# Kernel optimization log

Measured on AMD Instinct MI355X. Metric: run time of the kernel, lower is better.

## Reference

```python
import jax, jax.numpy as jnp
import numpy as np

D_MODEL = 1024
N_HEAD = 16
AGENT_NUM = 256


def setup_inputs() -> dict:
    key = jax.random.key(0)
    ks = jax.random.split(key, 11)
    B, S, D = 4, 2048, D_MODEL
    s = 1.0 / np.sqrt(D)
    return {
        "q": jax.random.normal(ks[0], (B, S, D), jnp.float32),
        "k": jax.random.normal(ks[1], (B, S, D), jnp.float32),
        "v": jax.random.normal(ks[2], (B, S, D), jnp.float32),
        "Wq": jax.random.normal(ks[3], (D, D), jnp.float32) * s,
        "bq": jnp.zeros((D,), jnp.float32),
        "Wk": jax.random.normal(ks[4], (D, D), jnp.float32) * s,
        "bk": jnp.zeros((D,), jnp.float32),
        "Wv": jax.random.normal(ks[5], (D, D), jnp.float32) * s,
        "bv": jnp.zeros((D,), jnp.float32),
        "Wo": jax.random.normal(ks[6], (D, D), jnp.float32) * s,
        "bo": jnp.zeros((D,), jnp.float32),
    }


def _split_heads(x, n_head):
    B, S, D = x.shape
    return x.reshape(B, S, n_head, D // n_head).transpose(0, 2, 1, 3)  # [B,H,S,d]


def reference(q, k, v, Wq, bq, Wk, bk, Wv, bv, Wo, bo):
    B, S, D = q.shape
    H, A = N_HEAD, AGENT_NUM
    d = D // H
    scale = 1.0 / jnp.sqrt(jnp.asarray(d, q.dtype))

    # QKV linear projections (torch Linear: x @ W.T + b)
    qh = _split_heads(q @ Wq.T + bq, H)  # [B,H,S,d]
    kh = _split_heads(k @ Wk.T + bk, H)
    vh = _split_heads(v @ Wv.T + bv, H)

    # Agent tokens: average-pool queries along sequence down to A tokens
    agent = qh.reshape(B, H, A, S // A, d).mean(axis=3)  # [B,H,A,d]

    # Stage 1: agents aggregate from keys/values (softmax over S)
    agent_attn = jax.nn.softmax(
        jnp.einsum("bhad,bhsd->bhas", agent, kh) * scale, axis=-1)  # [B,H,A,S]
    agent_v = jnp.einsum("bhas,bhsd->bhad", agent_attn, vh)  # [B,H,A,d]

    # Stage 2: queries attend to agent tokens (softmax over A)
    q_attn = jax.nn.softmax(
        jnp.einsum("bhsd,bhad->bhsa", qh, agent) * scale, axis=-1)  # [B,H,S,A]
    out_h = jnp.einsum("bhsa,bhad->bhsd", q_attn, agent_v)  # [B,H,S,d]

    # concat heads + output projection
    out = out_h.transpose(0, 2, 1, 3).reshape(B, S, D)
    out = out @ Wo.T + bo
    return out, q_attn
```

## Files before the change

kernel.cpp:

```cpp
#include <hip/hip_runtime.h>

constexpr int Bsz = 4, Ssz = 2048, Dsz = 1024, Hn = 16, dh = 64, An = 256;

typedef __attribute__((ext_vector_type(8))) short bf16x8;
typedef __attribute__((ext_vector_type(4))) float f32x4;

__device__ __forceinline__ unsigned short f2bf_rn(float f) {
    unsigned int u = __float_as_uint(f);
    return (unsigned short)((u + 0x7FFFu + ((u >> 16) & 1u)) >> 16);
}
__device__ __forceinline__ float bf2f(unsigned short h) {
    return __uint_as_float(((unsigned int)h) << 16);
}
__device__ __forceinline__ void bf_split(float f, unsigned short& hi, unsigned short& lo) {
    hi = f2bf_rn(f);
    lo = f2bf_rn(f - bf2f(hi));
}
__device__ __forceinline__ void gload16(const unsigned short* g, unsigned short* l) {
    __builtin_amdgcn_global_load_lds(
        (const __attribute__((address_space(1))) unsigned int*)g,
        (__attribute__((address_space(3))) unsigned int*)l, 16, 0, 0);
}
__device__ __forceinline__ bf16x8 gfrag(const unsigned short* g) {
    return *reinterpret_cast<const bf16x8*>(g);
}
__device__ __forceinline__ void make8(float4 a, float4 b, bf16x8& hi8, bf16x8& lo8) {
    float v[8] = {a.x, a.y, a.z, a.w, b.x, b.y, b.z, b.w};
    #pragma unroll
    for (int i = 0; i < 8; ++i) {
        unsigned short h, l;
        bf_split(v[i], h, l);
        hi8[i] = (short)h; lo8[i] = (short)l;
    }
}


template<int LOGC, int NISS>
__device__ __forceinline__ void stage_tile(const unsigned short* __restrict__ g, long rowStride,
                                           unsigned short* lbase, int t) {
    const int wid = t >> 6;
    #pragma unroll
    for (int i = 0; i < NISS; ++i) {
        int slot = i * 256 + t;
        int r = slot >> LOGC;
        int c = slot & ((1 << LOGC) - 1);
        int cs = (c ^ (r & 7)) & ((1 << LOGC) - 1);
        gload16(g + (long)r * rowStride + cs * 8, lbase + (i * 256 + wid * 64) * 8);
    }
}
template<int ROWLEN>
__device__ __forceinline__ bf16x8 fragR(const unsigned short* buf, int row, int ks, int lane) {
    int c = ks * 4 + (lane >> 4);
    int cs = (c ^ (row & 7)) & (ROWLEN / 8 - 1);
    return *reinterpret_cast<const bf16x8*>(buf + row * ROWLEN + cs * 8);
}

__global__ __launch_bounds__(256)
void split_kernel(const float* __restrict__ x, unsigned short* __restrict__ hi,
                  unsigned short* __restrict__ lo, int n4)
{
    int i = blockIdx.x * 256 + threadIdx.x;
    if (i >= n4) return;
    float4 v = reinterpret_cast<const float4*>(x)[i];
    ushort4 h, l;
    bf_split(v.x, h.x, l.x);
    bf_split(v.y, h.y, l.y);
    bf_split(v.z, h.z, l.z);
    bf_split(v.w, h.w, l.w);
    reinterpret_cast<ushort4*>(hi)[i] = h;
    reinterpret_cast<ushort4*>(lo)[i] = l;
}

#define MT 128
#define BKm 32

__device__ __forceinline__ bf16x8 lds_frag(const unsigned short* buf, int baseRow, int lane) {
    int row = baseRow + (lane & 15);
    int c = lane >> 4;
    int idx = row * 32 + ((c ^ ((row >> 1) & 3)) << 3);
    return *reinterpret_cast<const bf16x8*>(buf + idx);
}

template<int OMODE>
__global__ __launch_bounds__(256, 2)
void gemm_nt_mfma3(const unsigned short* __restrict__ Ahi, const unsigned short* __restrict__ Alo,
                   const unsigned short* __restrict__ Bhi, const unsigned short* __restrict__ Blo,
                   const float* __restrict__ bias, float* __restrict__ Cf,
                   unsigned short* __restrict__ Chi, unsigned short* __restrict__ Clo,
                   int K, int N)
{
    __shared__ unsigned short lds[4 * 4096];
    const int t = threadIdx.x;
    const int lane = t & 63, wid = t >> 6;
    const int wr = wid >> 1, wc = wid & 1;
    const int m0 = blockIdx.y * MT, n0 = blockIdx.x * MT;

    const int srow0 = t >> 2;
    const int x4 = t & 3;
    const int ldsBase0 = (wid * 64) * 8;
    const int ldsBase1 = (256 + wid * 64) * 8;

    f32x4 acc[4][4];
    #pragma unroll
    for (int i = 0; i < 4; ++i)
        #pragma unroll
        for (int j = 0; j < 4; ++j)
            acc[i][j] = f32x4{0.f, 0.f, 0.f, 0.f};

    const unsigned short* gA[2] = {Ahi, Alo};
    const unsigned short* gB[2] = {Bhi, Blo};

    for (int k0 = 0; k0 < K; k0 += BKm) {
        #pragma unroll
        for (int hb = 0; hb < 2; ++hb) {
            {
                const unsigned short* G = gA[hb];
                int r0 = srow0, r1 = srow0 + 64;
                int c0 = x4 ^ ((r0 >> 1) & 3);
                int c1 = x4 ^ ((r1 >> 1) & 3);
                gload16(G + (size_t)(m0 + r0) * K + k0 + c0 * 8, lds + hb * 4096 + ldsBase0);
                gload16(G + (size_t)(m0 + r1) * K + k0 + c1 * 8, lds + hb * 4096 + ldsBase1);
            }
            {
                const unsigned short* G = gB[hb];
                int r0 = srow0, r1 = srow0 + 64;
                int c0 = x4 ^ ((r0 >> 1) & 3);
                int c1 = x4 ^ ((r1 >> 1) & 3);
                gload16(G + (size_t)(n0 + r0) * K + k0 + c0 * 8, lds + (2 + hb) * 4096 + ldsBase0);
                gload16(G + (size_t)(n0 + r1) * K + k0 + c1 * 8, lds + (2 + hb) * 4096 + ldsBase1);
            }
        }
        __syncthreads();

        bf16x8 ah[4], al[4], bh[4], bl[4];
        #pragma unroll
        for (int mi = 0; mi < 4; ++mi) {
            ah[mi] = lds_frag(lds + 0 * 4096, wr * 64 + mi * 16, lane);
            al[mi] = lds_frag(lds + 1 * 4096, wr * 64 + mi * 16, lane);
        }
        #pragma unroll
        for (int ni = 0; ni < 4; ++ni) {
            bh[ni] = lds_frag(lds + 2 * 4096, wc * 64 + ni * 16, lane);
            bl[ni] = lds_frag(lds + 3 * 4096, wc * 64 + ni * 16, lane);
        }
        #pragma unroll
        for (int mi = 0; mi < 4; ++mi)
            #pragma unroll
            for (int ni = 0; ni < 4; ++ni) {
                acc[mi][ni] = __builtin_amdgcn_mfma_f32_16x16x32_bf16(ah[mi], bh[ni], acc[mi][ni], 0, 0, 0);
                acc[mi][ni] = __builtin_amdgcn_mfma_f32_16x16x32_bf16(ah[mi], bl[ni], acc[mi][ni], 0, 0, 0);
                acc[mi][ni] = __builtin_amdgcn_mfma_f32_16x16x32_bf16(al[mi], bh[ni], acc[mi][ni], 0, 0, 0);
            }
        __syncthreads();
    }

    #pragma unroll
    for (int mi = 0; mi < 4; ++mi) {
        #pragma unroll
        for (int ni = 0; ni < 4; ++ni) {
            const int n = n0 + wc * 64 + ni * 16 + (lane & 15);
            const float bval = bias[n];
            #pragma unroll
            for (int j = 0; j < 4; ++j) {
                const int m = m0 + wr * 64 + mi * 16 + ((lane >> 4) << 2) + j;
                float val = acc[mi][ni][j] + bval;
                if constexpr (OMODE == 0) {
                    Cf[(size_t)m * N + n] = val;
                } else {
                    const int b = m >> 11, s = m & (Ssz - 1);
                    const int h = n >> 6, c = n & (dh - 1);
                    size_t idx;
                    if constexpr (OMODE == 1)
                        idx = (((size_t)(b * Hn + h)) * Ssz + s) * dh + c;
                    else if constexpr (OMODE == 2)
                        idx = (((size_t)(b * Hn + h)) * dh + c) * Ssz + s;
                    else
                        idx = (size_t)(b * Hn + h) * 131072
                            + (((s >> 4) * 2 + (c >> 5)) << 9)
                            + (((c >> 3) & 3) << 7) + ((s & 15) << 3) + (c & 7);
                    unsigned short hi, lo;
                    bf_split(val, hi, lo);
                    Chi[idx] = hi; Clo[idx] = lo;
                }
            }
        }
    }
}

__global__ __launch_bounds__(256)
void pool_agent(const unsigned short* __restrict__ qh_hi, const unsigned short* __restrict__ qh_lo,
                unsigned short* __restrict__ ag_hi, unsigned short* __restrict__ ag_lo)
{
    const int idx = blockIdx.x * 256 + threadIdx.x;
    const int c = idx & (dh - 1);
    const int a = (idx >> 6) & (An - 1);
    const int bh = idx >> 14;
    const size_t base = (size_t)bh * 131072
        + (((a >> 1) * 2 + (c >> 5)) << 9) + (((c >> 3) & 3) << 7)
        + ((8 * (a & 1)) << 3) + (c & 7);
    float s = 0.f;
    #pragma unroll
    for (int j = 0; j < 8; ++j)
        s += bf2f(qh_hi[base + j * 8]) + bf2f(qh_lo[base + j * 8]);
    s *= 0.125f;
    unsigned short hi, lo;
    bf_split(s, hi, lo);
    const size_t oidx = (size_t)bh * 16384
        + (((a >> 4) * 2 + (c >> 5)) << 9) + (((c >> 3) & 3) << 7)
        + ((a & 15) << 3) + (c & 7);
    ag_hi[oidx] = hi; ag_lo[oidx] = lo;
}

__global__ __launch_bounds__(256, 3)
void flash1(const unsigned short* __restrict__ ag_hi, const unsigned short* __restrict__ ag_lo,
            const unsigned short* __restrict__ kh_hi, const unsigned short* __restrict__ kh_lo,
            const unsigned short* __restrict__ vt_hi_g, const unsigned short* __restrict__ vt_lo_g,
            unsigned short* __restrict__ avt_hi, unsigned short* __restrict__ avt_lo)
{
    __shared__ unsigned short lds[24576];
    unsigned short* kth = lds;
    unsigned short* ktl = lds + 4096;
    unsigned short* vth = lds + 8192;
    unsigned short* vtl = lds + 12288;
    const int t = threadIdx.x;
    const int lane = t & 63, w = t >> 6;
    const int al15 = lane & 15, hi4 = lane >> 4;
    unsigned short* pwh = lds + 16384 + w * 2048;
    unsigned short* pwl = pwh + 1024;

    const int bh = blockIdx.y;
    const int a0 = blockIdx.x * 64;

    bf16x8 bqh[2], bql[2];
    {
        const size_t abase = (size_t)bh * 16384 + (size_t)((a0 >> 4) + w) * 1024;
        #pragma unroll
        for (int ks = 0; ks < 2; ++ks) {
            bqh[ks] = gfrag(ag_hi + abase + ks * 512 + lane * 8);
            bql[ks] = gfrag(ag_lo + abase + ks * 512 + lane * 8);
        }
    }

    f32x4 O[4];
    #pragma unroll
    for (int i = 0; i < 4; ++i) O[i] = f32x4{0.f, 0.f, 0.f, 0.f};
    float m_run = -INFINITY, l_run = 0.f;

    for (int s0 = 0; s0 < Ssz; s0 += 64) {
        stage_tile<3, 2>(kh_hi + ((size_t)bh * Ssz + s0) * dh, dh, kth, t);
        stage_tile<3, 2>(kh_lo + ((size_t)bh * Ssz + s0) * dh, dh, ktl, t);
        stage_tile<3, 2>(vt_hi_g + (size_t)bh * dh * Ssz + s0, Ssz, vth, t);
        stage_tile<3, 2>(vt_lo_g + (size_t)bh * dh * Ssz + s0, Ssz, vtl, t);
        __syncthreads();

        f32x4 sc[4];
        #pragma unroll
        for (int si = 0; si < 4; ++si) sc[si] = f32x4{0.f, 0.f, 0.f, 0.f};
        #pragma unroll
        for (int si = 0; si < 4; ++si)
            #pragma unroll
            for (int ks = 0; ks < 2; ++ks) {
                bf16x8 ah = fragR<64>(kth, si * 16 + al15, ks, lane);
                bf16x8 al = fragR<64>(ktl, si * 16 + al15, ks, lane);
                sc[si] = __builtin_amdgcn_mfma_f32_16x16x32_bf16(ah, bqh[ks], sc[si], 0, 0, 0);
                sc[si] = __builtin_amdgcn_mfma_f32_16x16x32_bf16(ah, bql[ks], sc[si], 0, 0, 0);
                sc[si] = __builtin_amdgcn_mfma_f32_16x16x32_bf16(al, bqh[ks], sc[si], 0, 0, 0);
            }

        float tmax = -INFINITY;
        #pragma unroll
        for (int si = 0; si < 4; ++si)
            #pragma unroll
            for (int j = 0; j < 4; ++j) {
                sc[si][j] *= 0.125f;
                tmax = fmaxf(tmax, sc[si][j]);
            }
        tmax = fmaxf(tmax, __shfl_xor(tmax, 16));
        tmax = fmaxf(tmax, __shfl_xor(tmax, 32));
        float newm = fmaxf(m_run, tmax);
        float fac = __expf(m_run - newm);
        float tsum = 0.f;
        #pragma unroll
        for (int si = 0; si < 4; ++si)
            #pragma unroll
            for (int j = 0; j < 4; ++j) {
                float p = __expf(sc[si][j] - newm);
                sc[si][j] = p;
                tsum += p;
            }
        tsum += __shfl_xor(tsum, 16);
        tsum += __shfl_xor(tsum, 32);
        l_run = l_run * fac + tsum;
        m_run = newm;

        #pragma unroll
        for (int si = 0; si < 4; ++si) {
            ushort4 h4, l4;
            bf_split(sc[si][0], h4.x, l4.x);
            bf_split(sc[si][1], h4.y, l4.y);
            bf_split(sc[si][2], h4.z, l4.z);
            bf_split(sc[si][3], h4.w, l4.w);
            int baseS = si * 16 + (hi4 << 2);
            int addr = al15 * 64 + (baseS ^ ((al15 & 7) << 3));
            *reinterpret_cast<ushort4*>(pwh + addr) = h4;
            *reinterpret_cast<ushort4*>(pwl + addr) = l4;
        }

        float fj[4];
        #pragma unroll
        for (int j = 0; j < 4; ++j) fj[j] = __shfl(fac, (hi4 << 2) + j);
        #pragma unroll
        for (int di = 0; di < 4; ++di)
            #pragma unroll
            for (int j = 0; j < 4; ++j) O[di][j] *= fj[j];

        #pragma unroll
        for (int ks = 0; ks < 2; ++ks) {
            bf16x8 pah = fragR<64>(pwh, al15, ks, lane);
            bf16x8 pal = fragR<64>(pwl, al15, ks, lane);
            #pragma unroll
            for (int di = 0; di < 4; ++di) {
                bf16x8 vh = fragR<64>(vth, di * 16 + al15, ks, lane);
                bf16x8 vl = fragR<64>(vtl, di * 16 + al15, ks, lane);
                O[di] = __builtin_amdgcn_mfma_f32_16x16x32_bf16(pah, vh, O[di], 0, 0, 0);
                O[di] = __builtin_amdgcn_mfma_f32_16x16x32_bf16(pah, vl, O[di], 0, 0, 0);
                O[di] = __builtin_amdgcn_mfma_f32_16x16x32_bf16(pal, vh, O[di], 0, 0, 0);
            }
        }
        __syncthreads();
    }

    float lj[4];
    #pragma unroll
    for (int j = 0; j < 4; ++j) lj[j] = __shfl(l_run, (hi4 << 2) + j);
    #pragma unroll
    for (int di = 0; di < 4; ++di) {
        ushort4 h4, l4;
        #pragma unroll
        for (int j = 0; j < 4; ++j) {
            float val = O[di][j] / lj[j];
            unsigned short hi, lo;
            bf_split(val, hi, lo);
            ((unsigned short*)&h4)[j] = hi;
            ((unsigned short*)&l4)[j] = lo;
        }
        const size_t oidx = (size_t)bh * 16384
            + (size_t)(di * 8 + (a0 >> 5) + (w >> 1)) * 512
            + (size_t)((2 * w + (hi4 >> 1)) & 3) * 128
            + al15 * 8 + (hi4 & 1) * 4;
        *reinterpret_cast<ushort4*>(avt_hi + oidx) = h4;
        *reinterpret_cast<ushort4*>(avt_lo + oidx) = l4;
    }
}

__global__ __launch_bounds__(256, 2)
void flash2(const unsigned short* __restrict__ qh_hi, const unsigned short* __restrict__ qh_lo,
            const unsigned short* __restrict__ ag_hi, const unsigned short* __restrict__ ag_lo,
            const unsigned short* __restrict__ avt_hi, const unsigned short* __restrict__ avt_lo,
            float* __restrict__ q_attn,
            unsigned short* __restrict__ xo_hi, unsigned short* __restrict__ xo_lo)
{
    __shared__ float plds[4][4096];

    const int t = threadIdx.x, lane = t & 63, w = t >> 6;
    const int al15 = lane & 15, hi4 = lane >> 4;
    const int bh = blockIdx.y;
    const int s0 = blockIdx.x * 64;
    float* P = plds[w];

    bf16x8 bqh[2], bql[2];
    {
        const size_t qbase = (size_t)bh * 131072 + (size_t)((s0 >> 4) + w) * 1024;
        #pragma unroll
        for (int ks = 0; ks < 2; ++ks) {
            bqh[ks] = gfrag(qh_hi + qbase + ks * 512 + lane * 8);
            bql[ks] = gfrag(qh_lo + qbase + ks * 512 + lane * 8);
        }
    }

    const unsigned short* agh = ag_hi + (size_t)bh * 16384;
    const unsigned short* agl = ag_lo + (size_t)bh * 16384;
    f32x4 acc[16];
    #pragma unroll
    for (int ai = 0; ai < 16; ++ai) acc[ai] = f32x4{0.f, 0.f, 0.f, 0.f};
    #pragma unroll
    for (int ai = 0; ai < 16; ++ai)
        #pragma unroll
        for (int ks = 0; ks < 2; ++ks) {
            bf16x8 ah = gfrag(agh + (ai * 2 + ks) * 512 + lane * 8);
            bf16x8 al = gfrag(agl + (ai * 2 + ks) * 512 + lane * 8);
            acc[ai] = __builtin_amdgcn_mfma_f32_16x16x32_bf16(ah, bqh[ks], acc[ai], 0, 0, 0);
            acc[ai] = __builtin_amdgcn_mfma_f32_16x16x32_bf16(ah, bql[ks], acc[ai], 0, 0, 0);
            acc[ai] = __builtin_amdgcn_mfma_f32_16x16x32_bf16(al, bqh[ks], acc[ai], 0, 0, 0);
        }

    float mx = -INFINITY;
    #pragma unroll
    for (int ai = 0; ai < 16; ++ai)
        #pragma unroll
        for (int j = 0; j < 4; ++j) {
            acc[ai][j] *= 0.125f;
            mx = fmaxf(mx, acc[ai][j]);
        }
    mx = fmaxf(mx, __shfl_xor(mx, 16));
    mx = fmaxf(mx, __shfl_xor(mx, 32));
    float sum = 0.f;
    #pragma unroll
    for (int ai = 0; ai < 16; ++ai)
        #pragma unroll
        for (int j = 0; j < 4; ++j) {
            float p = __expf(acc[ai][j] - mx);
            acc[ai][j] = p;
            sum += p;
        }
    sum += __shfl_xor(sum, 16);
    sum += __shfl_xor(sum, 32);
    const float inv = 1.0f / sum;

    #pragma unroll
    for (int ai = 0; ai < 16; ++ai) {
        float4 o;
        o.x = acc[ai][0] * inv; o.y = acc[ai][1] * inv;
        o.z = acc[ai][2] * inv; o.w = acc[ai][3] * inv;
        int pos4 = (ai * 4 + hi4) ^ (al15 & 7);
        *reinterpret_cast<float4*>(P + al15 * 256 + pos4 * 4) = o;
    }

    {
        float* qbase = q_attn + ((size_t)bh * Ssz + s0 + w * 16) * An;
        #pragma unroll
        for (int r = 0; r < 16; ++r) {
            float4 f = *reinterpret_cast<const float4*>(P + r * 256 + ((lane ^ (r & 7)) * 4));
            *reinterpret_cast<float4*>(qbase + r * An + lane * 4) = f;
        }
    }

    const unsigned short* avh_b = avt_hi + (size_t)bh * 16384;
    const unsigned short* avl_b = avt_lo + (size_t)bh * 16384;
    f32x4 O[4];
    #pragma unroll
    for (int i = 0; i < 4; ++i) O[i] = f32x4{0.f, 0.f, 0.f, 0.f};
    #pragma unroll
    for (int ks = 0; ks < 8; ++ks) {
        int p4 = ks * 8 + hi4 * 2;
        float4 fa = *reinterpret_cast<const float4*>(P + al15 * 256 + ((p4 ^ (al15 & 7)) * 4));
        float4 fb = *reinterpret_cast<const float4*>(P + al15 * 256 + (((p4 + 1) ^ (al15 & 7)) * 4));
        bf16x8 pah, pal;
        make8(fa, fb, pah, pal);
        #pragma unroll
        for (int di = 0; di < 4; ++di) {
            bf16x8 avh = gfrag(avh_b + (di * 8 + ks) * 512 + lane * 8);
            bf16x8 avl = gfrag(avl_b + (di * 8 + ks) * 512 + lane * 8);
            O[di] = __builtin_amdgcn_mfma_f32_16x16x32_bf16(pah, avh, O[di], 0, 0, 0);
            O[di] = __builtin_amdgcn_mfma_f32_16x16x32_bf16(pah, avl, O[di], 0, 0, 0);
            O[di] = __builtin_amdgcn_mfma_f32_16x16x32_bf16(pal, avh, O[di], 0, 0, 0);
        }
    }

    const int b = bh >> 4, h = bh & (Hn - 1);
    #pragma unroll
    for (int di = 0; di < 4; ++di)
        #pragma unroll
        for (int j = 0; j < 4; ++j) {
            float val = O[di][j];
            int sG = s0 + w * 16 + (hi4 << 2) + j;
            int dfull = h * dh + di * 16 + al15;
            size_t idx = ((size_t)b * Ssz + sG) * Dsz + dfull;
            unsigned short hi, lo;
            bf_split(val, hi, lo);
            xo_hi[idx] = hi; xo_lo[idx] = lo;
        }
}

extern "C" void kernel_launch(void* const* d_in, const int* in_sizes, int n_in,
                              void* d_out, int out_size, void* d_ws, size_t ws_size,
                              hipStream_t stream)
{
    const float* q  = (const float*)d_in[0];
    const float* k  = (const float*)d_in[1];
    const float* v  = (const float*)d_in[2];
    const float* Wq = (const float*)d_in[3];
    const float* bq = (const float*)d_in[4];
    const float* Wk = (const float*)d_in[5];
    const float* bk = (const float*)d_in[6];
    const float* Wv = (const float*)d_in[7];
    const float* bv = (const float*)d_in[8];
    const float* Wo = (const float*)d_in[9];
    const float* bo = (const float*)d_in[10];

    constexpr size_t BSD = (size_t)Bsz * Ssz * Dsz;
    constexpr size_t DD  = (size_t)Dsz * Dsz;
    constexpr size_t AGD = (size_t)Bsz * Hn * An * dh;

    float* out    = (float*)d_out;
    float* q_attn = out + BSD;

    unsigned short* u = (unsigned short*)d_ws;
    unsigned short* x_hi   = u;
    unsigned short* x_lo   = x_hi + BSD;
    unsigned short* qh_hi  = x_lo + BSD;
    unsigned short* qh_lo  = qh_hi + BSD;
    unsigned short* kh_hi  = qh_lo + BSD;
    unsigned short* kh_lo  = kh_hi + BSD;
    unsigned short* vt_hi  = kh_lo + BSD;
    unsigned short* vt_lo  = vt_hi + BSD;
    unsigned short* w_hi   = vt_lo + BSD;
    unsigned short* w_lo   = w_hi + DD;
    unsigned short* ag_hi  = w_lo + DD;
    unsigned short* ag_lo  = ag_hi + AGD;
    unsigned short* avt_hi = ag_lo + AGD;
    unsigned short* avt_lo = avt_hi + AGD;

    const int M = Bsz * Ssz;
    dim3 gmfma(Dsz / MT, M / MT, 1);

    split_kernel<<<BSD / 1024, 256, 0, stream>>>(q, x_hi, x_lo, BSD / 4);
    split_kernel<<<DD / 1024, 256, 0, stream>>>(Wq, w_hi, w_lo, DD / 4);
    gemm_nt_mfma3<3><<<gmfma, 256, 0, stream>>>(x_hi, x_lo, w_hi, w_lo, bq, nullptr, qh_hi, qh_lo, Dsz, Dsz);
    split_kernel<<<BSD / 1024, 256, 0, stream>>>(k, x_hi, x_lo, BSD / 4);
    split_kernel<<<DD / 1024, 256, 0, stream>>>(Wk, w_hi, w_lo, DD / 4);
    gemm_nt_mfma3<1><<<gmfma, 256, 0, stream>>>(x_hi, x_lo, w_hi, w_lo, bk, nullptr, kh_hi, kh_lo, Dsz, Dsz);
    split_kernel<<<BSD / 1024, 256, 0, stream>>>(v, x_hi, x_lo, BSD / 4);
    split_kernel<<<DD / 1024, 256, 0, stream>>>(Wv, w_hi, w_lo, DD / 4);
    gemm_nt_mfma3<2><<<gmfma, 256, 0, stream>>>(x_hi, x_lo, w_hi, w_lo, bv, nullptr, vt_hi, vt_lo, Dsz, Dsz);

    pool_agent<<<AGD / 256, 256, 0, stream>>>(qh_hi, qh_lo, ag_hi, ag_lo);

    flash1<<<dim3(An / 64, Bsz * Hn), 256, 0, stream>>>(
        ag_hi, ag_lo, kh_hi, kh_lo, vt_hi, vt_lo, avt_hi, avt_lo);

    flash2<<<dim3(Ssz / 64, Bsz * Hn), 256, 0, stream>>>(
        qh_hi, qh_lo, ag_hi, ag_lo, avt_hi, avt_lo, q_attn, x_hi, x_lo);

    split_kernel<<<DD / 1024, 256, 0, stream>>>(Wo, w_hi, w_lo, DD / 4);
    gemm_nt_mfma3<0><<<gmfma, 256, 0, stream>>>(x_hi, x_lo, w_hi, w_lo, bo, out, nullptr, nullptr, Dsz, Dsz);
}
```

Before: 416.3 us.

## Fuse QKV projections into one pipelined K-concatenated split-bf16 GEMM

The three QKV GEMMs are replaced by a single launch. It folds the hi/lo split-bf16 trick into a K=3072 concatenated operand ([hi,hi,lo]·[hi,lo,hi]), so each k-step issues one MFMA instead of three. The new kernel uses 128x256 tiles, a three-stage LDS ring fed by global_load_lds with vmcnt-based waits, s_setprio around the MFMAs, and an XCD-aware block remap. Input and weight splitting are merged into two batched kernels, and all launches now use 1D grids with remapped block ids. The cost is three times the split-input footprint in workspace and larger operand reads per GEMM.

```diff
diff --git a/kernel.cpp b/kernel.cpp
--- a/kernel.cpp
+++ b/kernel.cpp
@@ -1,6 +1,12 @@
 #include <hip/hip_runtime.h>
 
 constexpr int Bsz = 4, Ssz = 2048, Dsz = 1024, Hn = 16, dh = 64, An = 256;
+constexpr size_t BSD = (size_t)Bsz * Ssz * Dsz;
+constexpr size_t DD  = (size_t)Dsz * Dsz;
+constexpr size_t AGD = (size_t)Bsz * Hn * An * dh;
+constexpr int KC = 3072;
+constexpr size_t ACD = (size_t)Bsz * Ssz * KC;
+constexpr size_t WCD = (size_t)Dsz * KC;
 
 typedef __attribute__((ext_vector_type(8))) short bf16x8;
 typedef __attribute__((ext_vector_type(4))) float f32x4;
@@ -33,7 +39,6 @@
         hi8[i] = (short)h; lo8[i] = (short)l;
     }
 }
-
 
 template<int LOGC, int NISS>
 __device__ __forceinline__ void stage_tile(const unsigned short* __restrict__ g, long rowStride,
@@ -56,19 +61,196 @@
 }
 
 __global__ __launch_bounds__(256)
-void split_kernel(const float* __restrict__ x, unsigned short* __restrict__ hi,
-                  unsigned short* __restrict__ lo, int n4)
-{
-    int i = blockIdx.x * 256 + threadIdx.x;
-    if (i >= n4) return;
-    float4 v = reinterpret_cast<const float4*>(x)[i];
+void split_inputs(const float* __restrict__ q, const float* __restrict__ k,
+                  const float* __restrict__ v,
+                  unsigned short* __restrict__ Aq, unsigned short* __restrict__ Ak,
+                  unsigned short* __restrict__ Av)
+{
+    const int job = blockIdx.y;
+    const float* src = (job == 0) ? q : (job == 1) ? k : v;
+    unsigned short* dst = (job == 0) ? Aq : (job == 1) ? Ak : Av;
+    int idx4 = blockIdx.x * 256 + threadIdx.x;
+    int row = idx4 >> 8;
+    int col = (idx4 & 255) * 4;
+    float4 v4 = reinterpret_cast<const float4*>(src)[idx4];
     ushort4 h, l;
-    bf_split(v.x, h.x, l.x);
-    bf_split(v.y, h.y, l.y);
-    bf_split(v.z, h.z, l.z);
-    bf_split(v.w, h.w, l.w);
-    reinterpret_cast<ushort4*>(hi)[i] = h;
-    reinterpret_cast<ushort4*>(lo)[i] = l;
+    bf_split(v4.x, h.x, l.x);
+    bf_split(v4.y, h.y, l.y);
+    bf_split(v4.z, h.z, l.z);
+    bf_split(v4.w, h.w, l.w);
+    unsigned short* rp = dst + (size_t)row * KC + col;
+    *reinterpret_cast<ushort4*>(rp)        = h;
+    *reinterpret_cast<ushort4*>(rp + 1024) = h;
+    *reinterpret_cast<ushort4*>(rp + 2048) = l;
+}
+
+__global__ __launch_bounds__(256)
+void split_weights(const float* __restrict__ Wq, const float* __restrict__ Wk,
+                   const float* __restrict__ Wv, const float* __restrict__ Wo,
+                   unsigned short* __restrict__ Wc,
+                   unsigned short* __restrict__ wo_hi, unsigned short* __restrict__ wo_lo)
+{
+    const int job = blockIdx.y;
+    const float* src = (job == 0) ? Wq : (job == 1) ? Wk : (job == 2) ? Wv : Wo;
+    int idx4 = blockIdx.x * 256 + threadIdx.x;
+    float4 v4 = reinterpret_cast<const float4*>(src)[idx4];
+    ushort4 h, l;
+    bf_split(v4.x, h.x, l.x);
+    bf_split(v4.y, h.y, l.y);
+    bf_split(v4.z, h.z, l.z);
+    bf_split(v4.w, h.w, l.w);
+    if (job < 3) {
+        int row = idx4 >> 8;
+        int col = (idx4 & 255) * 4;
+        unsigned short* rp = Wc + (size_t)job * WCD + (size_t)row * KC + col;
+        *reinterpret_cast<ushort4*>(rp)        = h;
+        *reinterpret_cast<ushort4*>(rp + 1024) = l;
+        *reinterpret_cast<ushort4*>(rp + 2048) = h;
+    } else {
+        reinterpret_cast<ushort4*>(wo_hi)[idx4] = h;
+        reinterpret_cast<ushort4*>(wo_lo)[idx4] = l;
+    }
+}
+
+__device__ __forceinline__ int frag_off(int row, int c4) {
+    int line = row >> 1;
+    int q = ((row & 1) << 2) + c4;
+    int qp = q ^ (line & 7);
+    return line * 64 + qp * 8;
+}
+
+__device__ __forceinline__ void stage_ab(const unsigned short* Abase, const unsigned short* Bbase,
+                                         const size_t* aoff, const size_t* boff, int koff,
+                                         unsigned short* abuf, unsigned short* bbuf, int wid) {
+    #pragma unroll
+    for (int i = 0; i < 2; ++i)
+        gload16(Abase + aoff[i] + koff, abuf + (i * 256 + wid * 64) * 8);
+    #pragma unroll
+    for (int i = 0; i < 4; ++i)
+        gload16(Bbase + boff[i] + koff, bbuf + (i * 256 + wid * 64) * 8);
+}
+
+__device__ __forceinline__ void kstep(const unsigned short* abuf, const unsigned short* bbuf,
+                                      f32x4 acc[8][4], int wn, int lane) {
+    const int al15 = lane & 15, c4 = lane >> 4;
+    bf16x8 bfr[4], afr[8];
+    #pragma unroll
+    for (int nf = 0; nf < 4; ++nf)
+        bfr[nf] = *reinterpret_cast<const bf16x8*>(bbuf + frag_off(wn * 64 + nf * 16 + al15, c4));
+    #pragma unroll
+    for (int mf = 0; mf < 8; ++mf)
+        afr[mf] = *reinterpret_cast<const bf16x8*>(abuf + frag_off(mf * 16 + al15, c4));
+    __builtin_amdgcn_s_setprio(1);
+    #pragma unroll
+    for (int mf = 0; mf < 8; ++mf)
+        #pragma unroll
+        for (int nf = 0; nf < 4; ++nf)
+            acc[mf][nf] = __builtin_amdgcn_mfma_f32_16x16x32_bf16(afr[mf], bfr[nf], acc[mf][nf], 0, 0, 0);
+    __builtin_amdgcn_s_setprio(0);
+}
+
+__global__ __launch_bounds__(256, 2)
+void gemm_qkv_pipe(const unsigned short* __restrict__ Aq, const unsigned short* __restrict__ Ak,
+                   const unsigned short* __restrict__ Av, const unsigned short* __restrict__ Wc,
+                   const float* __restrict__ bq, const float* __restrict__ bk, const float* __restrict__ bv,
+                   unsigned short* __restrict__ qh_hi, unsigned short* __restrict__ qh_lo,
+                   unsigned short* __restrict__ kh_hi, unsigned short* __restrict__ kh_lo,
+                   unsigned short* __restrict__ vt_hi, unsigned short* __restrict__ vt_lo)
+{
+    __shared__ unsigned short lds3[3 * 12288];
+    const int t = threadIdx.x, lane = t & 63, wid = t >> 6;
+    const int id = blockIdx.x;
+    const int z = id >> 8, rem = id & 255;
+    const int xcd = rem & 7, slot = rem >> 3;
+    const int m0 = (xcd * 8 + (slot >> 2)) * 128;
+    const int n0 = (slot & 3) * 256;
+
+    const unsigned short* A = (z == 0) ? Aq : (z == 1) ? Ak : Av;
+    const unsigned short* Abase = A + (size_t)m0 * KC;
+    const unsigned short* Bbase = Wc + (size_t)z * WCD + (size_t)n0 * KC;
+    const float* bias = (z == 0) ? bq : (z == 1) ? bk : bv;
+    unsigned short* Chi = (z == 0) ? qh_hi : (z == 1) ? kh_hi : vt_hi;
+    unsigned short* Clo = (z == 0) ? qh_lo : (z == 1) ? kh_lo : vt_lo;
+
+    size_t aoff[2], boff[4];
+    #pragma unroll
+    for (int i = 0; i < 2; ++i) {
+        int chk = i * 256 + t, line = chk >> 3, qp = chk & 7, q = qp ^ (line & 7);
+        aoff[i] = (size_t)(line * 2 + (q >> 2)) * KC + (q & 3) * 8;
+    }
+    #pragma unroll
+    for (int i = 0; i < 4; ++i) {
+        int chk = i * 256 + t, line = chk >> 3, qp = chk & 7, q = qp ^ (line & 7);
+        boff[i] = (size_t)(line * 2 + (q >> 2)) * KC + (q & 3) * 8;
+    }
+
+    f32x4 acc[8][4];
+    #pragma unroll
+    for (int i = 0; i < 8; ++i)
+        #pragma unroll
+        for (int j = 0; j < 4; ++j)
+            acc[i][j] = f32x4{0.f, 0.f, 0.f, 0.f};
+
+    stage_ab(Abase, Bbase, aoff, boff, 0,  lds3,         lds3 + 4096,          wid);
+    stage_ab(Abase, Bbase, aoff, boff, 32, lds3 + 12288, lds3 + 12288 + 4096,  wid);
+
+    constexpr int NT = KC / 32;
+    #pragma unroll 1
+    for (int kt = 0; kt < NT - 2; ++kt) {
+        unsigned short* sb = lds3 + ((kt + 2) % 3) * 12288;
+        stage_ab(Abase, Bbase, aoff, boff, (kt + 2) * 32, sb, sb + 4096, wid);
+        asm volatile("s_waitcnt vmcnt(12)" ::: "memory");
+        __builtin_amdgcn_s_barrier();
+        asm volatile("" ::: "memory");
+        const unsigned short* cb = lds3 + (kt % 3) * 12288;
+        kstep(cb, cb + 4096, acc, wid, lane);
+        asm volatile("" ::: "memory");
+        __builtin_amdgcn_s_barrier();
+    }
+    asm volatile("s_waitcnt vmcnt(6)" ::: "memory");
+    __builtin_amdgcn_s_barrier();
+    asm volatile("" ::: "memory");
+    {
+        const unsigned short* cb = lds3 + ((NT - 2) % 3) * 12288;
+        kstep(cb, cb + 4096, acc, wid, lane);
+    }
+    asm volatile("" ::: "memory");
+    __builtin_amdgcn_s_barrier();
+    asm volatile("s_waitcnt vmcnt(0)" ::: "memory");
+    __builtin_amdgcn_s_barrier();
+    asm volatile("" ::: "memory");
+    {
+        const unsigned short* cb = lds3 + ((NT - 1) % 3) * 12288;
+        kstep(cb, cb + 4096, acc, wid, lane);
+    }
+
+    #pragma unroll
+    for (int mf = 0; mf < 8; ++mf) {
+        #pragma unroll
+        for (int nf = 0; nf < 4; ++nf) {
+            const int n = n0 + wid * 64 + nf * 16 + (lane & 15);
+            const float bval = bias[n];
+            #pragma unroll
+            for (int j = 0; j < 4; ++j) {
+                const int m = m0 + mf * 16 + ((lane >> 4) << 2) + j;
+                float val = acc[mf][nf][j] + bval;
+                const int b = m >> 11, s = m & (Ssz - 1);
+                const int h = n >> 6, c = n & (dh - 1);
+                size_t idx;
+                if (z == 0)
+                    idx = (size_t)(b * Hn + h) * 131072
+                        + (((s >> 4) * 2 + (c >> 5)) << 9)
+                        + (((c >> 3) & 3) << 7) + ((s & 15) << 3) + (c & 7);
+                else if (z == 1)
+                    idx = (((size_t)(b * Hn + h)) * Ssz + s) * dh + c;
+                else
+                    idx = (((size_t)(b * Hn + h)) * dh + c) * Ssz + s;
+                unsigned short hi, lo;
+                bf_split(val, hi, lo);
+                Chi[idx] = hi; Clo[idx] = lo;
+            }
+        }
+    }
 }
 
 #define MT 128
@@ -81,36 +263,33 @@
     return *reinterpret_cast<const bf16x8*>(buf + idx);
 }
 
-template<int OMODE>
 __global__ __launch_bounds__(256, 2)
-void gemm_nt_mfma3(const unsigned short* __restrict__ Ahi, const unsigned short* __restrict__ Alo,
-                   const unsigned short* __restrict__ Bhi, const unsigned short* __restrict__ Blo,
-                   const float* __restrict__ bias, float* __restrict__ Cf,
-                   unsigned short* __restrict__ Chi, unsigned short* __restrict__ Clo,
-                   int K, int N)
-{
+void gemm_out(const unsigned short* __restrict__ Ahi_, const unsigned short* __restrict__ Alo_,
+              const unsigned short* __restrict__ Bhi_, const unsigned short* __restrict__ Blo_,
+              const float* __restrict__ bias, float* __restrict__ Cf)
+{
+    const int rem = blockIdx.x & 511;
+    const int xcd = rem & 7, slot = rem >> 3;
+    const int m0 = (xcd * 8 + (slot >> 3)) * MT;
+    const int n0 = (slot & 7) * MT;
+
     __shared__ unsigned short lds[4 * 4096];
     const int t = threadIdx.x;
     const int lane = t & 63, wid = t >> 6;
     const int wr = wid >> 1, wc = wid & 1;
-    const int m0 = blockIdx.y * MT, n0 = blockIdx.x * MT;
-
     const int srow0 = t >> 2;
     const int x4 = t & 3;
     const int ldsBase0 = (wid * 64) * 8;
     const int ldsBase1 = (256 + wid * 64) * 8;
-
     f32x4 acc[4][4];
     #pragma unroll
     for (int i = 0; i < 4; ++i)
         #pragma unroll
         for (int j = 0; j < 4; ++j)
             acc[i][j] = f32x4{0.f, 0.f, 0.f, 0.f};
-
-    const unsigned short* gA[2] = {Ahi, Alo};
-    const unsigned short* gB[2] = {Bhi, Blo};
-
-    for (int k0 = 0; k0 < K; k0 += BKm) {
+    const unsigned short* gA[2] = {Ahi_, Alo_};
+    const unsigned short* gB[2] = {Bhi_, Blo_};
+    for (int k0 = 0; k0 < Dsz; k0 += BKm) {
         #pragma unroll
         for (int hb = 0; hb < 2; ++hb) {
             {
@@ -118,20 +297,19 @@
                 int r0 = srow0, r1 = srow0 + 64;
                 int c0 = x4 ^ ((r0 >> 1) & 3);
                 int c1 = x4 ^ ((r1 >> 1) & 3);
-                gload16(G + (size_t)(m0 + r0) * K + k0 + c0 * 8, lds + hb * 4096 + ldsBase0);
-                gload16(G + (size_t)(m0 + r1) * K + k0 + c1 * 8, lds + hb * 4096 + ldsBase1);
+                gload16(G + (size_t)(m0 + r0) * Dsz + k0 + c0 * 8, lds + hb * 4096 + ldsBase0);
+                gload16(G + (size_t)(m0 + r1) * Dsz + k0 + c1 * 8, lds + hb * 4096 + ldsBase1);
             }
             {
                 const unsigned short* G = gB[hb];
                 int r0 = srow0, r1 = srow0 + 64;
                 int c0 = x4 ^ ((r0 >> 1) & 3);
                 int c1 = x4 ^ ((r1 >> 1) & 3);
-                gload16(G + (size_t)(n0 + r0) * K + k0 + c0 * 8, lds + (2 + hb) * 4096 + ldsBase0);
-                gload16(G + (size_t)(n0 + r1) * K + k0 + c1 * 8, lds + (2 + hb) * 4096 + ldsBase1);
+                gload16(G + (size_t)(n0 + r0) * Dsz + k0 + c0 * 8, lds + (2 + hb) * 4096 + ldsBase0);
+                gload16(G + (size_t)(n0 + r1) * Dsz + k0 + c1 * 8, lds + (2 + hb) * 4096 + ldsBase1);
             }
         }
         __syncthreads();
-
         bf16x8 ah[4], al[4], bh[4], bl[4];
         #pragma unroll
         for (int mi = 0; mi < 4; ++mi) {
@@ -163,25 +341,7 @@
             #pragma unroll
             for (int j = 0; j < 4; ++j) {
                 const int m = m0 + wr * 64 + mi * 16 + ((lane >> 4) << 2) + j;
-                float val = acc[mi][ni][j] + bval;
-                if constexpr (OMODE == 0) {
-                    Cf[(size_t)m * N + n] = val;
-                } else {
-                    const int b = m >> 11, s = m & (Ssz - 1);
-                    const int h = n >> 6, c = n & (dh - 1);
-                    size_t idx;
-                    if constexpr (OMODE == 1)
-                        idx = (((size_t)(b * Hn + h)) * Ssz + s) * dh + c;
-                    else if constexpr (OMODE == 2)
-                        idx = (((size_t)(b * Hn + h)) * dh + c) * Ssz + s;
-                    else
-                        idx = (size_t)(b * Hn + h) * 131072
-                            + (((s >> 4) * 2 + (c >> 5)) << 9)
-                            + (((c >> 3) & 3) << 7) + ((s & 15) << 3) + (c & 7);
-                    unsigned short hi, lo;
-                    bf_split(val, hi, lo);
-                    Chi[idx] = hi; Clo[idx] = lo;
-                }
+                Cf[(size_t)m * Dsz + n] = acc[mi][ni][j] + bval;
             }
         }
     }
@@ -228,8 +388,8 @@
     unsigned short* pwh = lds + 16384 + w * 2048;
     unsigned short* pwl = pwh + 1024;
 
-    const int bh = blockIdx.y;
-    const int a0 = blockIdx.x * 64;
+    const int bh = blockIdx.x & 63;
+    const int a0 = (blockIdx.x >> 6) * 64;
 
     bf16x8 bqh[2], bql[2];
     {
@@ -364,8 +524,8 @@
 
     const int t = threadIdx.x, lane = t & 63, w = t >> 6;
     const int al15 = lane & 15, hi4 = lane >> 4;
-    const int bh = blockIdx.y;
-    const int s0 = blockIdx.x * 64;
+    const int bh = blockIdx.x & 63;
+    const int s0 = (blockIdx.x >> 6) * 64;
     float* P = plds[w];
 
     bf16x8 bqh[2], bql[2];
@@ -488,50 +648,44 @@
     const float* Wo = (const float*)d_in[9];
     const float* bo = (const float*)d_in[10];
 
-    constexpr size_t BSD = (size_t)Bsz * Ssz * Dsz;
-    constexpr size_t DD  = (size_t)Dsz * Dsz;
-    constexpr size_t AGD = (size_t)Bsz * Hn * An * dh;
-
     float* out    = (float*)d_out;
     float* q_attn = out + BSD;
 
     unsigned short* u = (unsigned short*)d_ws;
-    unsigned short* x_hi   = u;
-    unsigned short* x_lo   = x_hi + BSD;
-    unsigned short* qh_hi  = x_lo + BSD;
-    unsigned short* qh_lo  = qh_hi + BSD;
-    unsigned short* kh_hi  = qh_lo + BSD;
-    unsigned short* kh_lo  = kh_hi + BSD;
-    unsigned short* vt_hi  = kh_lo + BSD;
-    unsigned short* vt_lo  = vt_hi + BSD;
-    unsigned short* w_hi   = vt_lo + BSD;
-    unsigned short* w_lo   = w_hi + DD;
-    unsigned short* ag_hi  = w_lo + DD;
-    unsigned short* ag_lo  = ag_hi + AGD;
+    unsigned short* Aq    = u;
+    unsigned short* Ak    = Aq + ACD;
+    unsigned short* Av    = Ak + ACD;
+    unsigned short* Wc    = Av + ACD;
+    unsigned short* wo_hi = Wc + 3 * WCD;
+    unsigned short* wo_lo = wo_hi + DD;
+    unsigned short* qh_hi = wo_lo + DD;
+    unsigned short* qh_lo = qh_hi + BSD;
+    unsigned short* kh_hi = qh_lo + BSD;
+    unsigned short* kh_lo = kh_hi + BSD;
+    unsigned short* vt_hi = kh_lo + BSD;
+    unsigned short* vt_lo = vt_hi + BSD;
+    unsigned short* xo_hi = vt_lo + BSD;
+    unsigned short* xo_lo = xo_hi + BSD;
+    unsigned short* ag_hi = xo_lo + BSD;
+    unsigned short* ag_lo = ag_hi + AGD;
     unsigned short* avt_hi = ag_lo + AGD;
     unsigned short* avt_lo = avt_hi + AGD;
 
-    const int M = Bsz * Ssz;
-    dim3 gmfma(Dsz / MT, M / MT, 1);
-
-    split_kernel<<<BSD / 1024, 256, 0, stream>>>(q, x_hi, x_lo, BSD / 4);
-    split_kernel<<<DD / 1024, 256, 0, stream>>>(Wq, w_hi, w_lo, DD / 4);
-    gemm_nt_mfma3<3><<<gmfma, 256, 0, stream>>>(x_hi, x_lo, w_hi, w_lo, bq, nullptr, qh_hi, qh_lo, Dsz, Dsz);
-    split_kernel<<<BSD / 1024, 256, 0, stream>>>(k, x_hi, x_lo, BSD / 4);
-    split_kernel<<<DD / 1024, 256, 0, stream>>>(Wk, w_hi, w_lo, DD / 4);
-    gemm_nt_mfma3<1><<<gmfma, 256, 0, stream>>>(x_hi, x_lo, w_hi, w_lo, bk, nullptr, kh_hi, kh_lo, Dsz, Dsz);
-    split_kernel<<<BSD / 1024, 256, 0, stream>>>(v, x_hi, x_lo, BSD / 4);
-    split_kernel<<<DD / 1024, 256, 0, stream>>>(Wv, w_hi, w_lo, DD / 4);
-    gemm_nt_mfma3<2><<<gmfma, 256, 0, stream>>>(x_hi, x_lo, w_hi, w_lo, bv, nullptr, vt_hi, vt_lo, Dsz, Dsz);
+    split_inputs<<<dim3(BSD / 1024, 3), 256, 0, stream>>>(q, k, v, Aq, Ak, Av);
+    split_weights<<<dim3(DD / 1024, 4), 256, 0, stream>>>(Wq, Wk, Wv, Wo, Wc, wo_hi, wo_lo);
+
+    gemm_qkv_pipe<<<768, 256, 0, stream>>>(
+        Aq, Ak, Av, Wc, bq, bk, bv,
+        qh_hi, qh_lo, kh_hi, kh_lo, vt_hi, vt_lo);
 
     pool_agent<<<AGD / 256, 256, 0, stream>>>(qh_hi, qh_lo, ag_hi, ag_lo);
 
-    flash1<<<dim3(An / 64, Bsz * Hn), 256, 0, stream>>>(
+    flash1<<<256, 256, 0, stream>>>(
         ag_hi, ag_lo, kh_hi, kh_lo, vt_hi, vt_lo, avt_hi, avt_lo);
 
-    flash2<<<dim3(Ssz / 64, Bsz * Hn), 256, 0, stream>>>(
-        qh_hi, qh_lo, ag_hi, ag_lo, avt_hi, avt_lo, q_attn, x_hi, x_lo);
-
-    split_kernel<<<DD / 1024, 256, 0, stream>>>(Wo, w_hi, w_lo, DD / 4);
-    gemm_nt_mfma3<0><<<gmfma, 256, 0, stream>>>(x_hi, x_lo, w_hi, w_lo, bo, out, nullptr, nullptr, Dsz, Dsz);
-}
+    flash2<<<2048, 256, 0, stream>>>(
+        qh_hi, qh_lo, ag_hi, ag_lo, avt_hi, avt_lo, q_attn, xo_hi, xo_lo);
+
+    gemm_out<<<512, 256, 0, stream>>>(
+        xo_hi, xo_lo, wo_hi, wo_lo, bo, out);
+}
```

Measured after the change: 477.8 us. 1.15x slower.
